# Performance work log

Measured on AMD Instinct MI355X. Metric: run time of the kernel, lower is better.

The kernel has to match this reference:

```python
import jax, jax.numpy as jnp
import numpy as np

N = 20000
E = 320000
IN_F = 128
HEADS = 8
OUT_F = 32
NEG_SLOPE = 0.2


def setup_inputs() -> dict:
    key = jax.random.key(0)
    k = jax.random.split(key, 8)
    x = jax.random.normal(k[0], (N, IN_F), dtype=jnp.float32)
    edge_index = jax.random.randint(k[1], (2, E), 0, N, dtype=jnp.int32)
    # Linear weights stored torch-style: [out, in]
    scale = 1.0 / np.sqrt(IN_F)
    W = jax.random.normal(k[2], (HEADS * OUT_F, IN_F), dtype=jnp.float32) * scale
    W1 = jax.random.normal(k[3], (HEADS * OUT_F, IN_F), dtype=jnp.float32) * scale
    W2 = jax.random.normal(k[4], (HEADS * OUT_F, IN_F), dtype=jnp.float32) * scale
    att = jax.random.normal(k[5], (1, HEADS, OUT_F), dtype=jnp.float32) * 0.1
    bias = jnp.zeros((HEADS * OUT_F,), dtype=jnp.float32)
    return {"x": x, "edge_index": edge_index, "W": W, "W1": W1, "W2": W2,
            "att": att, "bias": bias}


def reference(x, edge_index, W, W1, W2, att, bias):
    n, heads, out_f = x.shape[0], att.shape[1], att.shape[2]
    src, dst = edge_index[0], edge_index[1]

    # Node projections: [N, H, F]
    h_src = (x @ W1.T).reshape(n, heads, out_f)
    h_dst = (x @ W2.T).reshape(n, heads, out_f)
    values = (x @ W.T).reshape(n, heads, out_f)

    # Edge-wise GATv2 logits: a^T LeakyReLU(W1 h_i + W2 h_j)  -> [E, H]
    att_input = jax.nn.leaky_relu(h_src[src] + h_dst[dst], negative_slope=NEG_SLOPE)
    logits = jnp.einsum('ehf,hf->eh', att_input, att[0])

    # Segment softmax over incoming edges of each dst node (stable).
    seg_max = jax.ops.segment_max(logits, dst, num_segments=n)  # [N, H]
    exp_l = jnp.exp(logits - seg_max[dst])
    denom = jax.ops.segment_sum(exp_l, dst, num_segments=n)     # [N, H]
    weights = exp_l / denom[dst]                                # [E, H]

    # Weighted aggregation of source values into dst nodes.
    weighted = weights[:, :, None] * values[src]                # [E, H, F]
    out = jax.ops.segment_sum(weighted, dst, num_segments=n)    # [N, H, F]

    out = out.reshape(n, heads * out_f) + bias
    return out
```

## Files before the change

kernel.cpp:

```cpp
#include <hip/hip_runtime.h>
#include <math.h>

#define NN 20000
#define EE 320000
#define KF 128
#define HO 256
#define CAP 96

typedef __attribute__((ext_vector_type(8))) short short8;
typedef __attribute__((ext_vector_type(4))) float f32x4;
typedef __attribute__((ext_vector_type(2))) _Float16 half2_t;

static __device__ __forceinline__ unsigned short f2bf(float f) {
    union { float f; unsigned u; } v; v.f = f;
    unsigned u = v.u;
    u += 0x7fffu + ((u >> 16) & 1u);
    return (unsigned short)(u >> 16);
}
static __device__ __forceinline__ unsigned short f2h(float f) {
    _Float16 h = (_Float16)f;
    return __builtin_bit_cast(unsigned short, h);
}
static __device__ __forceinline__ float dot2f(half2_t a, half2_t b, float c) {
#if __has_builtin(__builtin_amdgcn_fdot2)
    return __builtin_amdgcn_fdot2(a, b, c, false);
#else
    return c + (float)a[0] * (float)b[0] + (float)a[1] * (float)b[1];
#endif
}

static __device__ __forceinline__ unsigned f_to_e3m4(float f) {
    const unsigned uf = __builtin_bit_cast(unsigned, f);
    float a = fabsf(f);
    a = fminf(fmaxf(a, 0.03125f), 7.75f);
    const unsigned ua = __builtin_bit_cast(unsigned, a);
    unsigned code = (ua - (122u << 23) + (1u << 18)) >> 19;
    code = (code > 127u) ? 127u : code;
    return ((uf >> 31) << 7) | code;
}
static __device__ __forceinline__ void e3m4x4_to_h2(unsigned w, half2_t& h01, half2_t& h23) {
    const unsigned u01 = __builtin_amdgcn_perm(0u, w, 0x0C010C00u);
    const unsigned u23 = __builtin_amdgcn_perm(0u, w, 0x0C030C02u);
    const unsigned r01 = ((u01 & 0x00800080u) << 8) | (((u01 & 0x007F007Fu) << 6) + 0x28002800u);
    const unsigned r23 = ((u23 & 0x00800080u) << 8) | (((u23 & 0x007F007Fu) << 6) + 0x28002800u);
    h01 = __builtin_bit_cast(half2_t, r01);
    h23 = __builtin_bit_cast(half2_t, r23);
}

__global__ __launch_bounds__(256) void prep_kernel(
    const float* __restrict__ x, const float* __restrict__ W0,
    const float* __restrict__ W1, const float* __restrict__ W2,
    unsigned short* __restrict__ xb, unsigned short* __restrict__ wb,
    int* __restrict__ cursor)
{
    const int b = blockIdx.x;
    const int t = threadIdx.x;
    if (b < 96) {
        const int m = b >> 5;
        const float* __restrict__ Wm = (m == 0) ? W0 : (m == 1) ? W1 : W2;
        int idx = (b & 31) * 1024 + t * 4;
        float4 v = *(const float4*)(Wm + idx);
        ushort4 o;
        o.x = f2bf(v.x); o.y = f2bf(v.y); o.z = f2bf(v.z); o.w = f2bf(v.w);
        *(ushort4*)(wb + (size_t)m * 32768 + idx) = o;
    } else if (b < 2596) {
        size_t i = (size_t)(b - 96) * 1024 + t * 4;
        float4 v = *(const float4*)(x + i);
        ushort4 o;
        o.x = f2bf(v.x); o.y = f2bf(v.y); o.z = f2bf(v.z); o.w = f2bf(v.w);
        *(ushort4*)(xb + i) = o;
    } else {
        int i = (b - 2596) * 256 + t;
        if (i < NN) cursor[i] = 0;
    }
}

__global__ __launch_bounds__(256, 4) void mid_kernel(
    const unsigned short* __restrict__ xb, const unsigned short* __restrict__ wb,
    unsigned char* __restrict__ hv8, unsigned short* __restrict__ hdst,
    const int* __restrict__ ei, int* __restrict__ cursor, int* __restrict__ csr_src)
{
    const int bid = blockIdx.x;
    if (bid < 313) {
        const int e0 = (bid * 256 + threadIdx.x) * 4;
        if (e0 + 3 < EE) {
            const int4 s4 = *(const int4*)(ei + e0);
            const int4 d4 = *(const int4*)(ei + EE + e0);
            const int p0 = atomicAdd(&cursor[d4.x], 1);
            const int p1 = atomicAdd(&cursor[d4.y], 1);
            const int p2 = atomicAdd(&cursor[d4.z], 1);
            const int p3 = atomicAdd(&cursor[d4.w], 1);
            if (p0 < CAP) csr_src[d4.x * CAP + p0] = s4.x;
            if (p1 < CAP) csr_src[d4.y * CAP + p1] = s4.y;
            if (p2 < CAP) csr_src[d4.z * CAP + p2] = s4.z;
            if (p3 < CAP) csr_src[d4.w * CAP + p3] = s4.w;
        } else {
            for (int e = e0; e < EE; ++e) {
                const int s = ei[e];
                const int d = ei[EE + e];
                const int pos = atomicAdd(&cursor[d], 1);
                if (pos < CAP) csr_src[d * CAP + pos] = s;
            }
        }
        return;
    }
    const int pb = bid - 313;
    const int m  = (pb < 313) ? 0 : (pb < 626) ? 1 : 2;
    const int bx = pb - m * 313;
    const unsigned short* __restrict__ Wm = wb + (size_t)m * 32768;

    const int w    = threadIdx.x >> 6;
    const int lane = threadIdx.x & 63;
    const int lr   = lane & 15;
    const int q    = lane >> 4;
    const int cb   = w * 64;

    short8 Bf[4][4];
#pragma unroll
    for (int nt = 0; nt < 4; ++nt)
#pragma unroll
        for (int ks = 0; ks < 4; ++ks)
            Bf[nt][ks] = *(const short8*)(Wm + (size_t)(cb + nt * 16 + lr) * KF + ks * 32 + q * 8);

    const int rb = bx * 64;

#pragma unroll
    for (int it = 0; it < 4; ++it) {
        const int r0 = rb + it * 16;

        short8 Af[4];
        const int arow = r0 + lr;
#pragma unroll
        for (int ks = 0; ks < 4; ++ks) {
            Af[ks] = (short8){0,0,0,0,0,0,0,0};
            if (arow < NN)
                Af[ks] = *(const short8*)(xb + (size_t)arow * KF + ks * 32 + q * 8);
        }

        f32x4 acc[4];
#pragma unroll
        for (int nt = 0; nt < 4; ++nt) acc[nt] = (f32x4){0.f, 0.f, 0.f, 0.f};

#pragma unroll
        for (int ks = 0; ks < 4; ++ks)
#pragma unroll
            for (int nt = 0; nt < 4; ++nt)
                acc[nt] = __builtin_amdgcn_mfma_f32_16x16x32_bf16(Af[ks], Bf[nt][ks], acc[nt], 0, 0, 0);

#pragma unroll
        for (int nt = 0; nt < 4; ++nt) {
            const int f = cb + nt * 16 + lr;
#pragma unroll
            for (int r = 0; r < 4; ++r) {
                const int row = r0 + q * 4 + r;
                if (row < NN) {
                    const float val = acc[nt][r];
                    if (m == 0)
                        *(unsigned short*)(hv8 + (size_t)row * 768 + 2 * f) = f2h(val);
                    else if (m == 1)
                        hv8[(size_t)row * 768 + 512 + f] = (unsigned char)f_to_e3m4(val);
                    else
                        hdst[(size_t)row * 256 + f] = f2h(val);
                }
            }
        }
    }
}

__global__ __launch_bounds__(128) void gat_kernel(
    const unsigned char* __restrict__ hv8, const unsigned short* __restrict__ hdst,
    const float* __restrict__ att, const float* __restrict__ bias,
    const int* __restrict__ cursor, const int* __restrict__ csr_src,
    float* __restrict__ out)
{
    const int w    = threadIdx.x >> 6;
    const int d    = blockIdx.x * 2 + w;
    const int lane = threadIdx.x & 63;
    const int col  = lane * 4;
    const int vo_v = lane * 8;
    const int vo_h = 512 + lane * 4;

    const float LOG2E = 1.4426950408889634f;
    const float4 av = *(const float4*)(att + col);
    const float s6 = 0.6f * LOG2E, s4 = 0.4f * LOG2E;
    const half2_t a6_01 = { (_Float16)(s6 * av.x), (_Float16)(s6 * av.y) };
    const half2_t a6_23 = { (_Float16)(s6 * av.z), (_Float16)(s6 * av.w) };
    const half2_t a4_01 = { (_Float16)(s4 * av.x), (_Float16)(s4 * av.y) };
    const half2_t a4_23 = { (_Float16)(s4 * av.z), (_Float16)(s4 * av.w) };
    const float4 b4 = *(const float4*)(bias + col);

    const uint2 hdb = *(const uint2*)(hdst + (size_t)d * HO + col);
    const half2_t hd01 = __builtin_bit_cast(half2_t, hdb.x);
    const half2_t hd23 = __builtin_bit_cast(half2_t, hdb.y);

    int deg = cursor[d];
    if (deg > CAP) deg = CAP;

    int sreg = (lane < deg) ? csr_src[d * CAP + lane] : 0;

    float l = 0.f;
    float o0 = 0.f, o1 = 0.f, o2 = 0.f, o3 = 0.f;

#define EDGE_CALC(V, H, VMUL)                                                 \
    {                                                                         \
        half2_t hs01, hs23;                                                   \
        e3m4x4_to_h2(H, hs01, hs23);                                          \
        half2_t z01 = hs01 + hd01;                                            \
        half2_t z23 = hs23 + hd23;                                            \
        const unsigned az01 = __builtin_bit_cast(unsigned, z01) & 0x7FFF7FFFu;\
        const unsigned az23 = __builtin_bit_cast(unsigned, z23) & 0x7FFF7FFFu;\
        float p = dot2f(a6_01, z01,                                           \
                  dot2f(a6_23, z23,                                           \
                  dot2f(a4_01, __builtin_bit_cast(half2_t, az01),             \
                  dot2f(a4_23, __builtin_bit_cast(half2_t, az23), 0.f))));    \
        p += __shfl_xor(p, 1); p += __shfl_xor(p, 2); p += __shfl_xor(p, 4);  \
        const float e = __builtin_amdgcn_exp2f(p) * (VMUL);                   \
        l += e;                                                               \
        const half2_t v01 = __builtin_bit_cast(half2_t, V.x);                 \
        const half2_t v23 = __builtin_bit_cast(half2_t, V.y);                 \
        o0 = fmaf((float)v01[0], e, o0);                                      \
        o1 = fmaf((float)v01[1], e, o1);                                      \
        o2 = fmaf((float)v23[0], e, o2);                                      \
        o3 = fmaf((float)v23[1], e, o3);                                      \
    }

    const int ng = (deg < 64) ? deg : 64;
    for (int i = 0; i < ng; i += 8) {
        float mm[8];
        uint2 V[8];
        unsigned H[8];
#pragma unroll
        for (int u = 0; u < 8; ++u) {
            const int s = __builtin_amdgcn_readlane(sreg, (i + u) & 63);
            mm[u] = (i + u < ng) ? 1.f : 0.f;
            const unsigned char* rp = hv8 + (size_t)s * 768;
            V[u] = *(const uint2*)(rp + vo_v);
            H[u] = *(const unsigned*)(rp + vo_h);
        }
#pragma unroll
        for (int u = 0; u < 8; ++u) EDGE_CALC(V[u], H[u], mm[u]);
    }
    for (int j = 64; j < deg; ++j) {
        const int s0 = csr_src[d * CAP + j];
        const unsigned char* rp = hv8 + (size_t)s0 * 768;
        const uint2 v = *(const uint2*)(rp + vo_v);
        const unsigned h = *(const unsigned*)(rp + vo_h);
        EDGE_CALC(v, h, 1.f);
    }
#undef EDGE_CALC

    const float inv = (deg > 0) ? 1.f / l : 0.f;
    float4 res;
    res.x = fmaf(o0, inv, b4.x);
    res.y = fmaf(o1, inv, b4.y);
    res.z = fmaf(o2, inv, b4.z);
    res.w = fmaf(o3, inv, b4.w);
    *(float4*)(out + (size_t)d * HO + col) = res;
}

extern "C" void kernel_launch(void* const* d_in, const int* in_sizes, int n_in,
                              void* d_out, int out_size, void* d_ws, size_t ws_size,
                              hipStream_t stream) {
    const float* x    = (const float*)d_in[0];
    const int*   ei   = (const int*)d_in[1];
    const float* W0   = (const float*)d_in[2];
    const float* W1   = (const float*)d_in[3];
    const float* W2   = (const float*)d_in[4];
    const float* att  = (const float*)d_in[5];
    const float* bias = (const float*)d_in[6];
    float* out = (float*)d_out;

    char* p = (char*)d_ws;
    unsigned char*  hv8  = (unsigned char*)p;  p += (size_t)NN * 768;
    unsigned short* hdst = (unsigned short*)p; p += (size_t)NN * HO * 2;
    unsigned short* xb   = (unsigned short*)p; p += (size_t)NN * KF * 2;
    unsigned short* wb   = (unsigned short*)p; p += (size_t)3 * 32768 * 2;
    int* cursor  = (int*)p; p += (size_t)NN * sizeof(int);
    int* csr_src = (int*)p; p += (size_t)NN * CAP * sizeof(int);

    prep_kernel<<<2675, 256, 0, stream>>>(x, W0, W1, W2, xb, wb, cursor);
    mid_kernel<<<1252, 256, 0, stream>>>(xb, wb, hv8, hdst, ei, cursor, csr_src);
    gat_kernel<<<NN / 2, 128, 0, stream>>>(hv8, hdst, att, bias, cursor, csr_src, out);
}
```

Before: 148.7 us.

## Fuse three projections per GEMM block and process two destinations per wave

The projection GEMM no longer gives each of the three weight matrices its own block. Each block now computes all three projections for 32 rows, which reuses the A-fragment rows in cache and cuts the grid from 939 to 626 GEMM blocks plus the 313 CSR blocks. The GAT kernel has each wave handle two destination nodes, dA and dA+10000, and issues their degree, CSR and hdst loads up front to overlap latency. The cost is a halved GAT grid, more serial work per wave, and unconditional csr_src reads for lanes beyond the degree.

Measured after the change: 194.5 us. 1.31x slower.

```diff
diff --git a/kernel.cpp b/kernel.cpp
--- a/kernel.cpp
+++ b/kernel.cpp
@@ -104,10 +104,8 @@
         }
         return;
     }
-    const int pb = bid - 313;
-    const int m  = (pb < 313) ? 0 : (pb < 626) ? 1 : 2;
-    const int bx = pb - m * 313;
-    const unsigned short* __restrict__ Wm = wb + (size_t)m * 32768;
+    const int bx = bid - 313;
+    const int rb = bx * 32;
 
     const int w    = threadIdx.x >> 6;
     const int lane = threadIdx.x & 63;
@@ -115,52 +113,54 @@
     const int q    = lane >> 4;
     const int cb   = w * 64;
 
-    short8 Bf[4][4];
-#pragma unroll
-    for (int nt = 0; nt < 4; ++nt)
-#pragma unroll
-        for (int ks = 0; ks < 4; ++ks)
-            Bf[nt][ks] = *(const short8*)(Wm + (size_t)(cb + nt * 16 + lr) * KF + ks * 32 + q * 8);
-
-    const int rb = bx * 64;
-
-#pragma unroll
-    for (int it = 0; it < 4; ++it) {
-        const int r0 = rb + it * 16;
-
-        short8 Af[4];
-        const int arow = r0 + lr;
-#pragma unroll
-        for (int ks = 0; ks < 4; ++ks) {
-            Af[ks] = (short8){0,0,0,0,0,0,0,0};
-            if (arow < NN)
-                Af[ks] = *(const short8*)(xb + (size_t)arow * KF + ks * 32 + q * 8);
-        }
-
-        f32x4 acc[4];
-#pragma unroll
-        for (int nt = 0; nt < 4; ++nt) acc[nt] = (f32x4){0.f, 0.f, 0.f, 0.f};
-
-#pragma unroll
-        for (int ks = 0; ks < 4; ++ks)
-#pragma unroll
-            for (int nt = 0; nt < 4; ++nt)
-                acc[nt] = __builtin_amdgcn_mfma_f32_16x16x32_bf16(Af[ks], Bf[nt][ks], acc[nt], 0, 0, 0);
-
-#pragma unroll
-        for (int nt = 0; nt < 4; ++nt) {
-            const int f = cb + nt * 16 + lr;
-#pragma unroll
-            for (int r = 0; r < 4; ++r) {
-                const int row = r0 + q * 4 + r;
-                if (row < NN) {
-                    const float val = acc[nt][r];
-                    if (m == 0)
-                        *(unsigned short*)(hv8 + (size_t)row * 768 + 2 * f) = f2h(val);
-                    else if (m == 1)
-                        hv8[(size_t)row * 768 + 512 + f] = (unsigned char)f_to_e3m4(val);
-                    else
-                        hdst[(size_t)row * 256 + f] = f2h(val);
+    for (int m = 0; m < 3; ++m) {
+        const unsigned short* __restrict__ Wm = wb + (size_t)m * 32768;
+
+        short8 Bf[4][4];
+#pragma unroll
+        for (int nt = 0; nt < 4; ++nt)
+#pragma unroll
+            for (int ks = 0; ks < 4; ++ks)
+                Bf[nt][ks] = *(const short8*)(Wm + (size_t)(cb + nt * 16 + lr) * KF + ks * 32 + q * 8);
+
+#pragma unroll
+        for (int it = 0; it < 2; ++it) {
+            const int r0 = rb + it * 16;
+
+            short8 Af[4];
+            const int arow = r0 + lr;
+#pragma unroll
+            for (int ks = 0; ks < 4; ++ks) {
+                Af[ks] = (short8){0,0,0,0,0,0,0,0};
+                if (arow < NN)
+                    Af[ks] = *(const short8*)(xb + (size_t)arow * KF + ks * 32 + q * 8);
+            }
+
+            f32x4 acc[4];
+#pragma unroll
+            for (int nt = 0; nt < 4; ++nt) acc[nt] = (f32x4){0.f, 0.f, 0.f, 0.f};
+
+#pragma unroll
+            for (int ks = 0; ks < 4; ++ks)
+#pragma unroll
+                for (int nt = 0; nt < 4; ++nt)
+                    acc[nt] = __builtin_amdgcn_mfma_f32_16x16x32_bf16(Af[ks], Bf[nt][ks], acc[nt], 0, 0, 0);
+
+#pragma unroll
+            for (int nt = 0; nt < 4; ++nt) {
+                const int f = cb + nt * 16 + lr;
+#pragma unroll
+                for (int r = 0; r < 4; ++r) {
+                    const int row = r0 + q * 4 + r;
+                    if (row < NN) {
+                        const float val = acc[nt][r];
+                        if (m == 0)
+                            *(unsigned short*)(hv8 + (size_t)row * 768 + 2 * f) = f2h(val);
+                        else if (m == 1)
+                            hv8[(size_t)row * 768 + 512 + f] = (unsigned char)f_to_e3m4(val);
+                        else
+                            hdst[(size_t)row * 256 + f] = f2h(val);
+                    }
                 }
             }
         }
@@ -174,11 +174,19 @@
     float* __restrict__ out)
 {
     const int w    = threadIdx.x >> 6;
-    const int d    = blockIdx.x * 2 + w;
+    const int dA   = blockIdx.x * 2 + w;
+    const int dB   = dA + 10000;
     const int lane = threadIdx.x & 63;
     const int col  = lane * 4;
     const int vo_v = lane * 8;
     const int vo_h = 512 + lane * 4;
+
+    int degA = cursor[dA];
+    int degB = cursor[dB];
+    const int svA = csr_src[dA * CAP + lane];
+    const int svB = csr_src[dB * CAP + lane];
+    const uint2 hdbA = *(const uint2*)(hdst + (size_t)dA * HO + col);
+    const uint2 hdbB = *(const uint2*)(hdst + (size_t)dB * HO + col);
 
     const float LOG2E = 1.4426950408889634f;
     const float4 av = *(const float4*)(att + col);
@@ -189,24 +197,15 @@
     const half2_t a4_23 = { (_Float16)(s4 * av.z), (_Float16)(s4 * av.w) };
     const float4 b4 = *(const float4*)(bias + col);
 
-    const uint2 hdb = *(const uint2*)(hdst + (size_t)d * HO + col);
-    const half2_t hd01 = __builtin_bit_cast(half2_t, hdb.x);
-    const half2_t hd23 = __builtin_bit_cast(half2_t, hdb.y);
-
-    int deg = cursor[d];
-    if (deg > CAP) deg = CAP;
-
-    int sreg = (lane < deg) ? csr_src[d * CAP + lane] : 0;
-
-    float l = 0.f;
-    float o0 = 0.f, o1 = 0.f, o2 = 0.f, o3 = 0.f;
-
-#define EDGE_CALC(V, H, VMUL)                                                 \
+    if (degA > CAP) degA = CAP;
+    if (degB > CAP) degB = CAP;
+
+#define EDGE_CALC(V, H, VMUL, HD01, HD23)                                     \
     {                                                                         \
         half2_t hs01, hs23;                                                   \
         e3m4x4_to_h2(H, hs01, hs23);                                          \
-        half2_t z01 = hs01 + hd01;                                            \
-        half2_t z23 = hs23 + hd23;                                            \
+        half2_t z01 = hs01 + HD01;                                            \
+        half2_t z23 = hs23 + HD23;                                            \
         const unsigned az01 = __builtin_bit_cast(unsigned, z01) & 0x7FFF7FFFu;\
         const unsigned az23 = __builtin_bit_cast(unsigned, z23) & 0x7FFF7FFFu;\
         float p = dot2f(a6_01, z01,                                           \
@@ -224,38 +223,53 @@
         o3 = fmaf((float)v23[1], e, o3);                                      \
     }
 
-    const int ng = (deg < 64) ? deg : 64;
-    for (int i = 0; i < ng; i += 8) {
-        float mm[8];
-        uint2 V[8];
-        unsigned H[8];
-#pragma unroll
-        for (int u = 0; u < 8; ++u) {
-            const int s = __builtin_amdgcn_readlane(sreg, (i + u) & 63);
-            mm[u] = (i + u < ng) ? 1.f : 0.f;
-            const unsigned char* rp = hv8 + (size_t)s * 768;
-            V[u] = *(const uint2*)(rp + vo_v);
-            H[u] = *(const unsigned*)(rp + vo_h);
-        }
-#pragma unroll
-        for (int u = 0; u < 8; ++u) EDGE_CALC(V[u], H[u], mm[u]);
-    }
-    for (int j = 64; j < deg; ++j) {
-        const int s0 = csr_src[d * CAP + j];
-        const unsigned char* rp = hv8 + (size_t)s0 * 768;
-        const uint2 v = *(const uint2*)(rp + vo_v);
-        const unsigned h = *(const unsigned*)(rp + vo_h);
-        EDGE_CALC(v, h, 1.f);
-    }
+#define PROCESS_DST(DD, DEG, SV, HD01, HD23)                                  \
+    {                                                                         \
+        const int sreg = (lane < (DEG)) ? (SV) : 0;                           \
+        float l = 0.f;                                                        \
+        float o0 = 0.f, o1 = 0.f, o2 = 0.f, o3 = 0.f;                         \
+        const int ng = ((DEG) < 64) ? (DEG) : 64;                             \
+        for (int i = 0; i < ng; i += 8) {                                     \
+            float mm[8];                                                      \
+            uint2 V[8];                                                       \
+            unsigned H[8];                                                    \
+            _Pragma("unroll")                                                 \
+            for (int u = 0; u < 8; ++u) {                                     \
+                const int s = __builtin_amdgcn_readlane(sreg, (i + u) & 63);  \
+                mm[u] = (i + u < ng) ? 1.f : 0.f;                             \
+                const unsigned char* rp = hv8 + (size_t)s * 768;              \
+                V[u] = *(const uint2*)(rp + vo_v);                            \
+                H[u] = *(const unsigned*)(rp + vo_h);                         \
+            }                                                                 \
+            _Pragma("unroll")                                                 \
+            for (int u = 0; u < 8; ++u) EDGE_CALC(V[u], H[u], mm[u], HD01, HD23); \
+        }                                                                     \
+        for (int j = 64; j < (DEG); ++j) {     \
+            const int s0 = csr_src[(DD) * CAP + j];                           \
+            const unsigned char* rp = hv8 + (size_t)s0 * 768;                 \
+            const uint2 v = *(const uint2*)(rp + vo_v);                       \
+            const unsigned h = *(const unsigned*)(rp + vo_h);                 \
+            EDGE_CALC(v, h, 1.f, HD01, HD23);                                 \
+        }                                                                     \
+        const float inv = ((DEG) > 0) ? 1.f / l : 0.f;                        \
+        float4 res;                                                           \
+        res.x = fmaf(o0, inv, b4.x);                                          \
+        res.y = fmaf(o1, inv, b4.y);                                          \
+        res.z = fmaf(o2, inv, b4.z);                                          \
+        res.w = fmaf(o3, inv, b4.w);                                          \
+        *(float4*)(out + (size_t)(DD) * HO + col) = res;                      \
+    }
+
+    const half2_t hdA01 = __builtin_bit_cast(half2_t, hdbA.x);
+    const half2_t hdA23 = __builtin_bit_cast(half2_t, hdbA.y);
+    const half2_t hdB01 = __builtin_bit_cast(half2_t, hdbB.x);
+    const half2_t hdB23 = __builtin_bit_cast(half2_t, hdbB.y);
+
+    PROCESS_DST(dA, degA, svA, hdA01, hdA23)
+    PROCESS_DST(dB, degB, svB, hdB01, hdB23)
+
+#undef PROCESS_DST
 #undef EDGE_CALC
-
-    const float inv = (deg > 0) ? 1.f / l : 0.f;
-    float4 res;
-    res.x = fmaf(o0, inv, b4.x);
-    res.y = fmaf(o1, inv, b4.y);
-    res.z = fmaf(o2, inv, b4.z);
-    res.w = fmaf(o3, inv, b4.w);
-    *(float4*)(out + (size_t)d * HO + col) = res;
 }
 
 extern "C" void kernel_launch(void* const* d_in, const int* in_sizes, int n_in,
@@ -279,6 +293,6 @@
     int* csr_src = (int*)p; p += (size_t)NN * CAP * sizeof(int);
 
     prep_kernel<<<2675, 256, 0, stream>>>(x, W0, W1, W2, xb, wb, cursor);
-    mid_kernel<<<1252, 256, 0, stream>>>(xb, wb, hv8, hdst, ei, cursor, csr_src);
-    gat_kernel<<<NN / 2, 128, 0, stream>>>(hv8, hdst, att, bias, cursor, csr_src, out);
-}
+    mid_kernel<<<939, 256, 0, stream>>>(xb, wb, hv8, hdst, ei, cursor, csr_src);
+    gat_kernel<<<NN / 4, 128, 0, stream>>>(hv8, hdst, att, bias, cursor, csr_src, out);
+}
```
